# Performance work log

Measured on AMD Instinct MI355X. Metric: run time of the kernel, lower is better.

Reference implementation:

```python
import jax, jax.numpy as jnp
import numpy as np

C_X = 768
NUM_HEAD = 16
QKV_DIM = C_X // NUM_HEAD
SEQ = 2048
NEG_INF = -1e9


def setup_inputs() -> dict:
    key = jax.random.key(0)
    ks = jax.random.split(key, 8)
    x = jax.random.normal(ks[0], (SEQ, C_X), dtype=jnp.float32)
    mask = jnp.ones((SEQ,), dtype=bool)
    pair_logits = jax.random.normal(ks[1], (NUM_HEAD, SEQ, SEQ), dtype=jnp.float32)
    s = 1.0 / np.sqrt(C_X)
    Wq = jax.random.normal(ks[2], (C_X, C_X), dtype=jnp.float32) * s
    bq = jax.random.normal(ks[3], (C_X,), dtype=jnp.float32) * 0.02
    Wk = jax.random.normal(ks[4], (C_X, C_X), dtype=jnp.float32) * s
    Wv = jax.random.normal(ks[5], (C_X, C_X), dtype=jnp.float32) * s
    Wg = jax.random.normal(ks[6], (C_X, C_X), dtype=jnp.float32) * s
    return {"x": x, "mask": mask, "pair_logits": pair_logits,
            "Wq": Wq, "bq": bq, "Wk": Wk, "Wv": Wv, "Wg": Wg}


def reference(x, mask, pair_logits, Wq, bq, Wk, Wv, Wg):
    S, C = x.shape
    H, D = NUM_HEAD, QKV_DIM
    scale = D ** -0.5
    # projections: q has bias, k/v/gating do not (matches nn.Linear flags)
    q = ((x @ Wq) + bq).reshape(S, H, D) * scale  # [S,H,D]
    k = (x @ Wk).reshape(S, H, D)
    v = (x @ Wv).reshape(S, H, D)
    logits = jnp.einsum('qhd,khd->hqk', q, k) + pair_logits  # [H,S,S]
    logits = jnp.where(mask[None, None, :], logits, NEG_INF)
    probs = jax.nn.softmax(logits, axis=-1)
    o = jnp.einsum('hqk,khd->qhd', probs, v).reshape(S, C)
    gate = jax.nn.sigmoid(x @ Wg)
    return gate * o
```

## Files before the change

### kernel.cpp

```cpp
#include <hip/hip_runtime.h>

#define SEQ 2048
#define CX 768
#define NH 16
#define HD 48
#define DP 64
#define NTOT 3584
#define QSCALE 0.14433756729740643f
#define LOG2E 1.4426950408889634f

typedef __attribute__((ext_vector_type(8))) __bf16 bfx8;
typedef __attribute__((ext_vector_type(8))) unsigned short usx8;
typedef __attribute__((ext_vector_type(4))) float f32x4;

__device__ __forceinline__ unsigned short f2bf(float f) {
  unsigned int u = __float_as_uint(f);
  u += 0x7FFFu + ((u >> 16) & 1u);
  return (unsigned short)(u >> 16);
}
__device__ __forceinline__ float bf2f(unsigned short u) {
  union { unsigned int i; float f; } v; v.i = ((unsigned int)u) << 16; return v.f;
}

__global__ void prep_wt(const float* __restrict__ Wq,
                        const float* __restrict__ Wk,
                        const float* __restrict__ Wv,
                        const float* __restrict__ Wg,
                        unsigned short* __restrict__ wt)
{
  __shared__ unsigned short T[64][65];
  const int nbase = blockIdx.x * 64;
  const int kk0 = blockIdx.y * 64;
  const float* W; int cbase, width;
  if (nbase < 1024)      { W = Wq; cbase = (nbase >> 6) * 48;          width = 48; }
  else if (nbase < 2048) { W = Wk; cbase = ((nbase - 1024) >> 6) * 48; width = 48; }
  else if (nbase < 2816) { W = Wv; cbase = nbase - 2048;               width = 64; }
  else                   { W = Wg; cbase = nbase - 2816;               width = 64; }
  const int tid = threadIdx.x;
  for (int e = tid; e < 4096; e += 256) {
    int r = e >> 6, cc = e & 63;
    T[r][cc] = (cc < width) ? f2bf(W[(kk0 + r) * CX + cbase + cc]) : (unsigned short)0;
  }
  __syncthreads();
  for (int e = tid; e < 4096; e += 256) {
    int nl = e >> 6, kl = e & 63;
    wt[(nbase + nl) * CX + kk0 + kl] = T[kl][nl];
  }
}

__global__ void prep_bias(const float* __restrict__ bq, float* __restrict__ bqp)
{
  int n = blockIdx.x * 256 + threadIdx.x;
  if (n < 1024) {
    int d = n & 63;
    bqp[n] = (d < 48) ? bq[(n >> 6) * 48 + d] : 0.f;
  }
}

__global__ __launch_bounds__(256) void proj_gemm(
    const float* __restrict__ x, const unsigned short* __restrict__ wt,
    const float* __restrict__ bqp,
    unsigned short* __restrict__ qf, unsigned short* __restrict__ kf,
    unsigned short* __restrict__ vt, unsigned short* __restrict__ gnat)
{
  __shared__ unsigned short As[128 * 40];
  __shared__ unsigned short Bs[128 * 40];
  const int tid = threadIdx.x;
  const int wave = tid >> 6, lane = tid & 63;
  const int ln = lane & 15, quad = lane >> 4;
  const int row0 = blockIdx.x * 128, col0 = blockIdx.y * 128;
  const int wm = (wave & 1) * 64, wn = (wave >> 1) * 64;
  const int srow = tid >> 1, skb = (tid & 1) * 16;

  f32x4 acc[4][4] = {};

  const float* xp = x + (row0 + srow) * CX + skb;
  const unsigned short* wtp = wt + (col0 + srow) * CX + skb;

  for (int k0 = 0; k0 < CX; k0 += 32) {
    float4 f0 = *(const float4*)(xp + k0);
    float4 f1 = *(const float4*)(xp + k0 + 4);
    float4 f2 = *(const float4*)(xp + k0 + 8);
    float4 f3 = *(const float4*)(xp + k0 + 12);
    usx8 a0, a1;
    a0[0]=f2bf(f0.x); a0[1]=f2bf(f0.y); a0[2]=f2bf(f0.z); a0[3]=f2bf(f0.w);
    a0[4]=f2bf(f1.x); a0[5]=f2bf(f1.y); a0[6]=f2bf(f1.z); a0[7]=f2bf(f1.w);
    a1[0]=f2bf(f2.x); a1[1]=f2bf(f2.y); a1[2]=f2bf(f2.z); a1[3]=f2bf(f2.w);
    a1[4]=f2bf(f3.x); a1[5]=f2bf(f3.y); a1[6]=f2bf(f3.z); a1[7]=f2bf(f3.w);
    *(usx8*)&As[srow * 40 + skb]     = a0;
    *(usx8*)&As[srow * 40 + skb + 8] = a1;
    *(usx8*)&Bs[srow * 40 + skb]     = *(const usx8*)(wtp + k0);
    *(usx8*)&Bs[srow * 40 + skb + 8] = *(const usx8*)(wtp + k0 + 8);
    __syncthreads();
    bfx8 a[4], b[4];
#pragma unroll
    for (int mt = 0; mt < 4; ++mt)
      a[mt] = __builtin_bit_cast(bfx8, *(const usx8*)&As[(wm + mt * 16 + ln) * 40 + quad * 8]);
#pragma unroll
    for (int nt = 0; nt < 4; ++nt)
      b[nt] = __builtin_bit_cast(bfx8, *(const usx8*)&Bs[(wn + nt * 16 + ln) * 40 + quad * 8]);
#pragma unroll
    for (int mt = 0; mt < 4; ++mt)
#pragma unroll
      for (int nt = 0; nt < 4; ++nt)
        acc[mt][nt] = __builtin_amdgcn_mfma_f32_16x16x32_bf16(a[mt], b[nt], acc[mt][nt], 0, 0, 0);
    __syncthreads();
  }

#pragma unroll
  for (int mt = 0; mt < 4; ++mt) {
#pragma unroll
    for (int nt = 0; nt < 4; ++nt) {
      const int n = col0 + wn + nt * 16 + ln;
#pragma unroll
      for (int i = 0; i < 4; ++i) {
        const int s = row0 + wm + mt * 16 + quad * 4 + i;
        float v = acc[mt][nt][i];
        if (n < 1024) {
          qf[((n >> 6) * SEQ + s) * DP + (n & 63)] = f2bf((v + bqp[n]) * QSCALE);
        } else if (n < 2048) {
          const int n2 = n - 1024;
          kf[((n2 >> 6) * SEQ + s) * DP + (n2 & 63)] = f2bf(v);
        } else if (n < 2816) {
          vt[(n - 2048) * SEQ + s] = f2bf(v);
        } else {
          gnat[s * CX + (n - 2816)] = f2bf(1.f / (1.f + __builtin_amdgcn_exp2f(-v * LOG2E)));
        }
      }
    }
  }
}

struct KvTile {
  float plv[4][4];
  bfx8  kfr[4][2];
  bfx8  vfr[3][2];
};

__device__ __forceinline__ void load_tile(KvTile& T, int kv0,
    const unsigned short* __restrict__ kh, const unsigned short* __restrict__ vh,
    const float* __restrict__ plr, int ln, int quad)
{
#pragma unroll
  for (int nt = 0; nt < 4; ++nt) {
    const unsigned short* kp = kh + (kv0 + nt * 16 + ln) * DP + quad * 8;
    T.kfr[nt][0] = __builtin_bit_cast(bfx8, *(const usx8*)kp);
    T.kfr[nt][1] = __builtin_bit_cast(bfx8, *(const usx8*)(kp + 32));
  }
#pragma unroll
  for (int dt = 0; dt < 3; ++dt) {
    const unsigned short* vp = vh + (dt * 16 + ln) * SEQ + kv0 + quad * 8;
    T.vfr[dt][0] = __builtin_bit_cast(bfx8, *(const usx8*)vp);
    T.vfr[dt][1] = __builtin_bit_cast(bfx8, *(const usx8*)(vp + 32));
  }
#pragma unroll
  for (int nt = 0; nt < 4; ++nt)
#pragma unroll
    for (int i = 0; i < 4; ++i)
      T.plv[nt][i] = plr[(size_t)i * SEQ + kv0 + nt * 16 + ln];
}

__global__ __launch_bounds__(64, 2) void attn(
    const unsigned short* __restrict__ qf, const unsigned short* __restrict__ kf,
    const unsigned short* __restrict__ vt, const float* __restrict__ pl,
    const unsigned short* __restrict__ gnat, float* __restrict__ out)
{
  __shared__ unsigned short P[16][72];
  const int h = blockIdx.x;
  const int qr0 = blockIdx.y * 16;
  const int lane = threadIdx.x;
  const int ln = lane & 15, quad = lane >> 4;

  const unsigned short* qh = qf + h * SEQ * DP;
  const unsigned short* kh = kf + h * SEQ * DP;
  const unsigned short* vh = vt + h * HD * SEQ;
  const int prow = qr0 + quad * 4;
  const float* plr = pl + (size_t)h * SEQ * SEQ + (size_t)prow * SEQ;

  const bfx8 aq0 = __builtin_bit_cast(bfx8, *(const usx8*)(qh + (qr0 + ln) * DP + quad * 8));
  const bfx8 aq1 = __builtin_bit_cast(bfx8, *(const usx8*)(qh + (qr0 + ln) * DP + 32 + quad * 8));

  f32x4 oacc[3] = {};
  float m_i[4], l_i[4];
#pragma unroll
  for (int i = 0; i < 4; ++i) { m_i[i] = -1.0e30f; l_i[i] = 0.f; }

  auto process = [&](const KvTile& T) {
    f32x4 s4[4] = {};
#pragma unroll
    for (int nt = 0; nt < 4; ++nt) {
      s4[nt] = __builtin_amdgcn_mfma_f32_16x16x32_bf16(aq0, T.kfr[nt][0], s4[nt], 0, 0, 0);
      s4[nt] = __builtin_amdgcn_mfma_f32_16x16x32_bf16(aq1, T.kfr[nt][1], s4[nt], 0, 0, 0);
    }
#pragma unroll
    for (int nt = 0; nt < 4; ++nt)
#pragma unroll
      for (int i = 0; i < 4; ++i)
        s4[nt][i] += T.plv[nt][i];

#pragma unroll
    for (int i = 0; i < 4; ++i) {
      float mx = fmaxf(fmaxf(s4[0][i], s4[1][i]), fmaxf(s4[2][i], s4[3][i]));
#pragma unroll
      for (int off = 1; off < 16; off <<= 1)
        mx = fmaxf(mx, __shfl_xor(mx, off, 64));
      const float mnew = fmaxf(m_i[i], mx);
      const float alpha = __builtin_amdgcn_exp2f((m_i[i] - mnew) * LOG2E);
      m_i[i] = mnew;
      float sum = 0.f;
#pragma unroll
      for (int nt = 0; nt < 4; ++nt) {
        float p = __builtin_amdgcn_exp2f((s4[nt][i] - mnew) * LOG2E);
        s4[nt][i] = p;
        sum += p;
      }
#pragma unroll
      for (int off = 1; off < 16; off <<= 1)
        sum += __shfl_xor(sum, off, 64);
      l_i[i] = l_i[i] * alpha + sum;
      oacc[0][i] *= alpha; oacc[1][i] *= alpha; oacc[2][i] *= alpha;
    }

#pragma unroll
    for (int nt = 0; nt < 4; ++nt)
#pragma unroll
      for (int i = 0; i < 4; ++i)
        P[quad * 4 + i][nt * 16 + ln] = f2bf(s4[nt][i]);

    asm volatile("s_waitcnt lgkmcnt(0)" ::: "memory");
    __builtin_amdgcn_sched_barrier(0);

    bfx8 ap0 = __builtin_bit_cast(bfx8, *(const usx8*)&P[ln][quad * 8]);
    bfx8 ap1 = __builtin_bit_cast(bfx8, *(const usx8*)&P[ln][32 + quad * 8]);

#pragma unroll
    for (int dt = 0; dt < 3; ++dt) {
      oacc[dt] = __builtin_amdgcn_mfma_f32_16x16x32_bf16(ap0, T.vfr[dt][0], oacc[dt], 0, 0, 0);
      oacc[dt] = __builtin_amdgcn_mfma_f32_16x16x32_bf16(ap1, T.vfr[dt][1], oacc[dt], 0, 0, 0);
    }
  };

  KvTile A, B;
  load_tile(A, 0, kh, vh, plr, ln, quad);
  for (int kv0 = 0; kv0 < SEQ; kv0 += 128) {
    load_tile(B, kv0 + 64, kh, vh, plr, ln, quad);
    process(A);
    const int nx = (kv0 + 128 < SEQ) ? kv0 + 128 : SEQ - 64;
    load_tile(A, nx, kh, vh, plr, ln, quad);
    process(B);
  }

#pragma unroll
  for (int dt = 0; dt < 3; ++dt) {
#pragma unroll
    for (int i = 0; i < 4; ++i) {
      const int srow = prow + i;
      const int c = h * HD + dt * 16 + ln;
      const float o = oacc[dt][i] / l_i[i];
      const float g = bf2f(gnat[srow * CX + c]);
      out[srow * CX + c] = g * o;
    }
  }
}

extern "C" void kernel_launch(void* const* d_in, const int* in_sizes, int n_in,
                              void* d_out, int out_size, void* d_ws, size_t ws_size,
                              hipStream_t stream)
{
  const float* x  = (const float*)d_in[0];
  const float* pl = (const float*)d_in[2];
  const float* Wq = (const float*)d_in[3];
  const float* bq = (const float*)d_in[4];
  const float* Wk = (const float*)d_in[5];
  const float* Wv = (const float*)d_in[6];
  const float* Wg = (const float*)d_in[7];
  float* out = (float*)d_out;

  unsigned short* wt   = (unsigned short*)d_ws;
  float* bqp           = (float*)(wt + NTOT * CX);
  unsigned short* qf   = (unsigned short*)(bqp + 1024);
  unsigned short* kf   = qf + NH * SEQ * DP;
  unsigned short* vt   = kf + NH * SEQ * DP;
  unsigned short* gnat = vt + CX * SEQ;

  prep_wt<<<dim3(56, 12), 256, 0, stream>>>(Wq, Wk, Wv, Wg, wt);
  prep_bias<<<4, 256, 0, stream>>>(bq, bqp);
  proj_gemm<<<dim3(16, 28), 256, 0, stream>>>(x, wt, bqp, qf, kf, vt, gnat);
  attn<<<dim3(16, 128), 64, 0, stream>>>(qf, kf, vt, pl, gnat, out);
}
```

Before: 504.7 us.

## Split attention KV range across four blocks and merge partials in a combine kernel

Turns the attention kernel into a split-KV (flash-decoding style) kernel. Each block now covers a quarter of the key sequence and writes an unnormalized output plus its row max and sum to workspace, and a new combine kernel rescales and merges the four partials and applies the gate. Launch bounds go from 2 to 4 waves per SIMD. The aim is to raise parallelism and latency hiding for a kernel that is bound by streaming pair_logits. In exchange it adds partial-output write and read traffic, an extra launch, and register pressure from the tighter bound. A fallback keeps the unsplit path when the workspace is too small.

Result: slower. 734.1 us (+45.4%).

```diff
diff --git a/kernel.cpp b/kernel.cpp
--- a/kernel.cpp
+++ b/kernel.cpp
@@ -6,6 +6,7 @@
 #define HD 48
 #define DP 64
 #define NTOT 3584
+#define NKV 4
 #define QSCALE 0.14433756729740643f
 #define LOG2E 1.4426950408889634f
 
@@ -160,14 +161,19 @@
       T.plv[nt][i] = plr[(size_t)i * SEQ + kv0 + nt * 16 + ln];
 }
 
-__global__ __launch_bounds__(64, 2) void attn(
+template<int KVLEN, bool PARTIAL>
+__global__ __launch_bounds__(64, 4) void attn_k(
     const unsigned short* __restrict__ qf, const unsigned short* __restrict__ kf,
     const unsigned short* __restrict__ vt, const float* __restrict__ pl,
-    const unsigned short* __restrict__ gnat, float* __restrict__ out)
+    const unsigned short* __restrict__ gnat, float* __restrict__ out,
+    float* __restrict__ op, float2* __restrict__ ml)
 {
   __shared__ unsigned short P[16][72];
   const int h = blockIdx.x;
   const int qr0 = blockIdx.y * 16;
+  const int z = blockIdx.z;
+  const int kvbeg = z * KVLEN;
+  const int kvend = kvbeg + KVLEN;
   const int lane = threadIdx.x;
   const int ln = lane & 15, quad = lane >> 4;
 
@@ -241,26 +247,66 @@
   };
 
   KvTile A, B;
-  load_tile(A, 0, kh, vh, plr, ln, quad);
-  for (int kv0 = 0; kv0 < SEQ; kv0 += 128) {
+  load_tile(A, kvbeg, kh, vh, plr, ln, quad);
+  for (int kv0 = kvbeg; kv0 < kvend; kv0 += 128) {
     load_tile(B, kv0 + 64, kh, vh, plr, ln, quad);
     process(A);
-    const int nx = (kv0 + 128 < SEQ) ? kv0 + 128 : SEQ - 64;
+    const int nx = (kv0 + 128 < kvend) ? kv0 + 128 : kvend - 64;
     load_tile(A, nx, kh, vh, plr, ln, quad);
     process(B);
   }
 
-#pragma unroll
-  for (int dt = 0; dt < 3; ++dt) {
-#pragma unroll
-    for (int i = 0; i < 4; ++i) {
-      const int srow = prow + i;
-      const int c = h * HD + dt * 16 + ln;
-      const float o = oacc[dt][i] / l_i[i];
-      const float g = bf2f(gnat[srow * CX + c]);
-      out[srow * CX + c] = g * o;
-    }
-  }
+  if constexpr (PARTIAL) {
+#pragma unroll
+    for (int dt = 0; dt < 3; ++dt)
+#pragma unroll
+      for (int i = 0; i < 4; ++i)
+        op[(size_t)((z * NH + h) * SEQ + prow + i) * HD + dt * 16 + ln] = oacc[dt][i];
+    if (ln == 0) {
+#pragma unroll
+      for (int i = 0; i < 4; ++i)
+        ml[(z * NH + h) * SEQ + prow + i] = make_float2(m_i[0 + i], l_i[0 + i]);
+    }
+  } else {
+#pragma unroll
+    for (int dt = 0; dt < 3; ++dt) {
+#pragma unroll
+      for (int i = 0; i < 4; ++i) {
+        const int srow = prow + i;
+        const int c = h * HD + dt * 16 + ln;
+        const float o = oacc[dt][i] / l_i[i];
+        const float g = bf2f(gnat[srow * CX + c]);
+        out[srow * CX + c] = g * o;
+      }
+    }
+  }
+}
+
+__global__ __launch_bounds__(256) void combine_k(
+    const float* __restrict__ op, const float2* __restrict__ ml,
+    const unsigned short* __restrict__ gnat, float* __restrict__ out)
+{
+  const int idx = blockIdx.x * 256 + threadIdx.x;
+  const int s = idx / CX, c = idx - s * CX;
+  const int h = c / HD, d = c - h * HD;
+  float m[NKV], l[NKV], o[NKV];
+#pragma unroll
+  for (int z = 0; z < NKV; ++z) {
+    float2 e = ml[(z * NH + h) * SEQ + s];
+    m[z] = e.x; l[z] = e.y;
+    o[z] = op[(size_t)((z * NH + h) * SEQ + s) * HD + d];
+  }
+  float M = m[0];
+#pragma unroll
+  for (int z = 1; z < NKV; ++z) M = fmaxf(M, m[z]);
+  float L = 0.f, O = 0.f;
+#pragma unroll
+  for (int z = 0; z < NKV; ++z) {
+    const float w = __builtin_amdgcn_exp2f((m[z] - M) * LOG2E);
+    L += l[z] * w;
+    O += o[z] * w;
+  }
+  out[idx] = bf2f(gnat[idx]) * O / L;
 }
 
 extern "C" void kernel_launch(void* const* d_in, const int* in_sizes, int n_in,
@@ -282,9 +328,21 @@
   unsigned short* kf   = qf + NH * SEQ * DP;
   unsigned short* vt   = kf + NH * SEQ * DP;
   unsigned short* gnat = vt + CX * SEQ;
+  float* op            = (float*)(gnat + SEQ * CX);
+  float2* ml           = (float2*)(op + (size_t)NKV * NH * SEQ * HD);
+
+  const size_t need = (size_t)((char*)(ml + (size_t)NKV * NH * SEQ) - (char*)d_ws);
 
   prep_wt<<<dim3(56, 12), 256, 0, stream>>>(Wq, Wk, Wv, Wg, wt);
   prep_bias<<<4, 256, 0, stream>>>(bq, bqp);
   proj_gemm<<<dim3(16, 28), 256, 0, stream>>>(x, wt, bqp, qf, kf, vt, gnat);
-  attn<<<dim3(16, 128), 64, 0, stream>>>(qf, kf, vt, pl, gnat, out);
-}
+
+  if (ws_size >= need) {
+    attn_k<SEQ / NKV, true><<<dim3(NH, SEQ / 16, NKV), 64, 0, stream>>>(
+        qf, kf, vt, pl, gnat, out, op, ml);
+    combine_k<<<SEQ * CX / 256, 256, 0, stream>>>(op, ml, gnat, out);
+  } else {
+    attn_k<SEQ, false><<<dim3(NH, SEQ / 16, 1), 64, 0, stream>>>(
+        qf, kf, vt, pl, gnat, out, nullptr, nullptr);
+  }
+}
```
